# Optimization experiments

Hardware: AMD Instinct MI355X
Metric: run time of the kernel (lower is better)

## Reference

```python
import jax, jax.numpy as jnp
import numpy as np

GROUPS = 32
EPS = 1e-3  # keras GroupNormalization default epsilon


def setup_inputs() -> dict:
    key = jax.random.key(0)
    ks = jax.random.split(key, 7)
    B, H, W, C = 16, 32, 32, 512
    inputs = jax.random.normal(ks[0], (B, H, W, C), dtype=jnp.float32)
    gamma = jnp.ones((C,), dtype=jnp.float32)
    beta = jnp.zeros((C,), dtype=jnp.float32)
    # EinsumDense 'bhwc,cae->bhwae', output last dims (C,3), bias axes 'ae'
    W_qkv = jax.random.normal(ks[1], (C, C, 3), dtype=jnp.float32) / np.sqrt(C)
    b_qkv = jnp.zeros((C, 3), dtype=jnp.float32)
    # EinsumDense 'bhwc,cd->bhwd', bias axes 'd'
    W_out = jax.random.normal(ks[2], (C, C), dtype=jnp.float32) / np.sqrt(C)
    b_out = jnp.zeros((C,), dtype=jnp.float32)
    return {
        "inputs": inputs,
        "gamma": gamma,
        "beta": beta,
        "W_qkv": W_qkv,
        "b_qkv": b_qkv,
        "W_out": W_out,
        "b_out": b_out,
    }


def group_norm(x, gamma, beta):
    B, H, W, C = x.shape
    g = GROUPS
    xr = x.reshape(B, H, W, g, C // g)
    mean = jnp.mean(xr, axis=(1, 2, 4), keepdims=True)
    var = jnp.var(xr, axis=(1, 2, 4), keepdims=True)
    xn = (xr - mean) * jax.lax.rsqrt(var + EPS)
    return xn.reshape(B, H, W, C) * gamma + beta


def reference(inputs, gamma, beta, W_qkv, b_qkv, W_out, b_out):
    B, H, W, C = inputs.shape
    scale = C ** (-0.5)
    x = group_norm(inputs, gamma, beta)
    # QKV projection: bhwc,cae->bhwae  (+ bias over 'ae')
    qkv = jnp.einsum("bhwc,cae->bhwae", x, W_qkv) + b_qkv
    q, k, v = qkv[..., 0], qkv[..., 1], qkv[..., 2]  # each [B,H,W,C]
    # full spatial attention: [B,H,W,H,W]
    attn = jnp.einsum("bhwc,btlc->bhwtl", q, k) * scale
    attn = attn.reshape(B, H, W, H * W)
    attn = jax.nn.softmax(attn, axis=-1)
    attn = attn.reshape(B, H, W, H, W)
    out = jnp.einsum("bhwtl,btlc->bhwc", attn, v)
    out = jnp.einsum("bhwc,cd->bhwd", out, W_out) + b_out
    return inputs + out
```

## Files before the change

### kernel.cpp

```cpp
#include <hip/hip_runtime.h>
#include <hip/hip_bf16.h>

#define NB    16
#define SP    1024
#define NC    512
#define NG    32
#define MTOT  (NB*SP)
#define EPSV  1e-3f
#define SCALE 0.04419417382415922f

using f32x4   = __attribute__((ext_vector_type(4))) float;
using short8  = __attribute__((ext_vector_type(8))) short;
using short4v = __attribute__((ext_vector_type(4))) short;
using bf16x8v = __attribute__((ext_vector_type(8))) __bf16;

__device__ __forceinline__ unsigned short f2bf(float f) {
  union { float f; unsigned int u; } x; x.f = f;
  unsigned int u = x.u;
  unsigned int r = (u + 0x7FFFu + ((u >> 16) & 1u)) >> 16;
  return (unsigned short)r;
}
__device__ __forceinline__ float bf2f(unsigned short b) {
  union { unsigned int u; float f; } x; x.u = ((unsigned int)b) << 16;
  return x.f;
}

#define GLOAD_LDS16(g, l)                                                     \
  __builtin_amdgcn_global_load_lds(                                           \
      (const __attribute__((address_space(1))) void*)(g),                     \
      (__attribute__((address_space(3))) void*)(l), 16, 0, 0)

__global__ __launch_bounds__(256) void gn_stats_k(const float* __restrict__ x,
                                                  float2* __restrict__ stats) {
  int bg = blockIdx.x;
  int b = bg >> 5, g = bg & 31;
  int tid = threadIdx.x;
  int c = tid & 15, s0 = tid >> 4;
  const float* base = x + (long)b * SP * NC + g * 16 + c;
  float s = 0.f, ss = 0.f;
  for (int sp = s0; sp < SP; sp += 16) {
    float v = base[(long)sp * NC];
    s += v; ss += v * v;
  }
  for (int o = 32; o > 0; o >>= 1) { s += __shfl_xor(s, o); ss += __shfl_xor(ss, o); }
  __shared__ float rs[4], rss[4];
  int lane = tid & 63, wv = tid >> 6;
  if (lane == 0) { rs[wv] = s; rss[wv] = ss; }
  __syncthreads();
  if (tid == 0) {
    float S = rs[0] + rs[1] + rs[2] + rs[3];
    float SS = rss[0] + rss[1] + rss[2] + rss[3];
    float mean = S * (1.f / 16384.f);
    float var  = SS * (1.f / 16384.f) - mean * mean;
    stats[bg] = make_float2(mean, rsqrtf(var + EPSV));
  }
}

__global__ __launch_bounds__(256) void gn_apply_k(const float* __restrict__ x,
                                                  const float2* __restrict__ stats,
                                                  const float* __restrict__ gamma,
                                                  const float* __restrict__ beta,
                                                  unsigned short* __restrict__ xn) {
  long t = (long)blockIdx.x * 256 + threadIdx.x;
  long base = t * 8;
  int c = (int)(base & 511);
  int b = (int)(base >> 19);
  float2 st = stats[b * NG + (c >> 4)];
  f32x4 v0 = *reinterpret_cast<const f32x4*>(x + base);
  f32x4 v1 = *reinterpret_cast<const f32x4*>(x + base + 4);
  f32x4 g0 = *reinterpret_cast<const f32x4*>(gamma + c);
  f32x4 g1 = *reinterpret_cast<const f32x4*>(gamma + c + 4);
  f32x4 b0 = *reinterpret_cast<const f32x4*>(beta + c);
  f32x4 b1 = *reinterpret_cast<const f32x4*>(beta + c + 4);
  short8 o;
  #pragma unroll
  for (int q = 0; q < 4; ++q) {
    float sc = st.y * g0[q];
    o[q] = (short)f2bf(v0[q] * sc + (b0[q] - st.x * sc));
  }
  #pragma unroll
  for (int q = 0; q < 4; ++q) {
    float sc = st.y * g1[q];
    o[q + 4] = (short)f2bf(v1[q] * sc + (b1[q] - st.x * sc));
  }
  *reinterpret_cast<short8*>(xn + base) = o;
}

__global__ __launch_bounds__(256) void pack_wqkv_k(const float* __restrict__ W,
                                                   const float* __restrict__ bq,
                                                   unsigned short* __restrict__ Wp,
                                                   float* __restrict__ bp) {
  int idx = blockIdx.x * 256 + threadIdx.x;
  int n = idx >> 9, c = idx & 511;
  int e = n >> 9, a = n & 511;
  Wp[idx] = f2bf(W[((long)c * 512 + a) * 3 + e]);
  if (idx < 1536) {
    int e2 = idx >> 9, a2 = idx & 511;
    bp[idx] = bq[a2 * 3 + e2];
  }
}

__global__ __launch_bounds__(256) void pack_wout_k(const float* __restrict__ W,
                                                   unsigned short* __restrict__ Wp) {
  int idx = blockIdx.x * 256 + threadIdx.x;
  int n = idx >> 9, c = idx & 511;
  Wp[idx] = f2bf(W[(long)c * 512 + n]);
}

__global__ void transpose_v_k(const unsigned short* __restrict__ qkv,
                              unsigned short* __restrict__ vT) {
  __shared__ unsigned short t[32][33];
  int bs = blockIdx.x, bc = blockIdx.y, b = blockIdx.z;
  int tx = threadIdx.x, ty = threadIdx.y;
  #pragma unroll
  for (int k = 0; k < 4; ++k) {
    int s = bs * 32 + ty + k * 8, c = bc * 32 + tx;
    t[ty + k * 8][tx] = qkv[((long)b * SP + s) * 1536 + 1024 + c];
  }
  __syncthreads();
  #pragma unroll
  for (int k = 0; k < 4; ++k) {
    int c = bc * 32 + ty + k * 8, s = bs * 32 + tx;
    vT[((long)b * NC + c) * SP + s] = t[tx][ty + k * 8];
  }
}

__global__ __launch_bounds__(256) void softmax_k(unsigned short* __restrict__ S) {
  long row = blockIdx.x;
  unsigned short* r = S + row * 1024;
  int tid = threadIdx.x, lane = tid & 63, wv = tid >> 6;
  short4v raw = *reinterpret_cast<const short4v*>(r + tid * 4);
  float v[4];
  #pragma unroll
  for (int q = 0; q < 4; ++q) v[q] = bf2f((unsigned short)raw[q]);
  float m = fmaxf(fmaxf(v[0], v[1]), fmaxf(v[2], v[3]));
  for (int o = 32; o > 0; o >>= 1) m = fmaxf(m, __shfl_xor(m, o));
  __shared__ float wm[4], ws[4];
  if (lane == 0) wm[wv] = m;
  __syncthreads();
  float rmax = fmaxf(fmaxf(wm[0], wm[1]), fmaxf(wm[2], wm[3]));
  float e[4]; float ssum = 0.f;
  #pragma unroll
  for (int q = 0; q < 4; ++q) { e[q] = __expf(v[q] - rmax); ssum += e[q]; }
  for (int o = 32; o > 0; o >>= 1) ssum += __shfl_xor(ssum, o);
  if (lane == 0) ws[wv] = ssum;
  __syncthreads();
  float inv = 1.f / (ws[0] + ws[1] + ws[2] + ws[3]);
  short4v pv;
  #pragma unroll
  for (int q = 0; q < 4; ++q) pv[q] = (short)f2bf(e[q] * inv);
  *reinterpret_cast<short4v*>(r + tid * 4) = pv;
}

template <int EPI>
__global__ __launch_bounds__(256) void gemm_tn(
    const unsigned short* __restrict__ Ap, long strideA, int lda,
    const unsigned short* __restrict__ Bp, long strideB, int ldb,
    void* __restrict__ Op, long strideO, int ldo,
    const float* __restrict__ bias, const float* __restrict__ residual,
    int K, float scale) {
  __shared__ unsigned short As[128 * 32];
  __shared__ unsigned short Bs[128 * 32];
  const int tid = threadIdx.x;
  const int lane = tid & 63, wv = tid >> 6;

  const int nwg  = gridDim.x * gridDim.y;
  const int flat = blockIdx.y * gridDim.x + blockIdx.x;
  const int w    = (flat & 7) * (nwg >> 3) + (flat >> 3);
  const int bn = (w % gridDim.x) * 128;
  const int bm = (w / gridDim.x) * 128;
  const int z = blockIdx.z;
  const unsigned short* Ag = Ap + (long)z * strideA;
  const unsigned short* Bg = Bp + (long)z * strideB;

  const int srow = lane >> 2;
  const int scol = (lane & 3) * 8;
  const int wm = (wv >> 1) * 64, wn = (wv & 1) * 64;
  const int lrow = lane & 15, lk = (lane >> 4) * 8;

  f32x4 acc[4][4] = {};
  for (int kt = 0; kt < K; kt += 32) {
    #pragma unroll
    for (int it = 0; it < 2; ++it) {
      int chunk = it * 4 + wv;
      int row = chunk * 16 + srow;
      GLOAD_LDS16(Ag + (long)(bm + row) * lda + kt + scol, As + chunk * 512);
      GLOAD_LDS16(Bg + (long)(bn + row) * ldb + kt + scol, Bs + chunk * 512);
    }
    __syncthreads();

    short8 afr[4], bfr[4];
    #pragma unroll
    for (int i = 0; i < 4; ++i)
      afr[i] = *reinterpret_cast<const short8*>(&As[(wm + i * 16 + lrow) * 32 + lk]);
    #pragma unroll
    for (int j = 0; j < 4; ++j)
      bfr[j] = *reinterpret_cast<const short8*>(&Bs[(wn + j * 16 + lrow) * 32 + lk]);
    #pragma unroll
    for (int i = 0; i < 4; ++i)
      #pragma unroll
      for (int j = 0; j < 4; ++j)
        acc[i][j] = __builtin_amdgcn_mfma_f32_16x16x32_bf16(
            __builtin_bit_cast(bf16x8v, afr[i]),
            __builtin_bit_cast(bf16x8v, bfr[j]), acc[i][j], 0, 0, 0);
    __syncthreads();
  }

  const int colb = bn + wn + (lane & 15);
  #pragma unroll
  for (int i = 0; i < 4; ++i) {
    #pragma unroll
    for (int r = 0; r < 4; ++r) {
      int rowg = bm + wm + i * 16 + (lane >> 4) * 4 + r;
      #pragma unroll
      for (int j = 0; j < 4; ++j) {
        int colg = colb + j * 16;
        float v = acc[i][j][r];
        if (EPI == 0) {
          v += bias[colg];
          ((unsigned short*)Op)[(long)z * strideO + (long)rowg * ldo + colg] = f2bf(v);
        } else if (EPI == 2) {
          ((unsigned short*)Op)[(long)z * strideO + (long)rowg * ldo + colg] = f2bf(v * scale);
        } else {
          v += bias[colg] + residual[(long)rowg * ldo + colg];
          ((float*)Op)[(long)rowg * ldo + colg] = v;
        }
      }
    }
  }
}

extern "C" void kernel_launch(void* const* d_in, const int* in_sizes, int n_in,
                              void* d_out, int out_size, void* d_ws, size_t ws_size,
                              hipStream_t stream) {
  const float* x     = (const float*)d_in[0];
  const float* gamma = (const float*)d_in[1];
  const float* beta  = (const float*)d_in[2];
  const float* Wqkv  = (const float*)d_in[3];
  const float* bqkv  = (const float*)d_in[4];
  const float* Wout  = (const float*)d_in[5];
  const float* bout  = (const float*)d_in[6];
  float* out = (float*)d_out;

  char* ws = (char*)d_ws;
  float2*         stats = (float2*)(ws + 0);
  unsigned short* wqkvP = (unsigned short*)(ws + 4096);
  float*          bqP   = (float*)(ws + 1576960);
  unsigned short* woutT = (unsigned short*)(ws + 1583104);
  unsigned short* qkv   = (unsigned short*)(ws + 2107392);
  unsigned short* vT    = (unsigned short*)(ws + 52439040);
  unsigned short* Sbuf  = (unsigned short*)(ws + 69216256);
  unsigned short* attn  = (unsigned short*)(ws + 136325120);
  unsigned short* xn    = (unsigned short*)(ws + 153102336);

  gn_stats_k<<<512, 256, 0, stream>>>(x, stats);
  gn_apply_k<<<4096, 256, 0, stream>>>(x, stats, gamma, beta, xn);
  pack_wqkv_k<<<3072, 256, 0, stream>>>(Wqkv, bqkv, wqkvP, bqP);
  pack_wout_k<<<1024, 256, 0, stream>>>(Wout, woutT);

  gemm_tn<0><<<dim3(12, 128, 1), 256, 0, stream>>>(
      xn, 0L, NC, wqkvP, 0L, NC, qkv, 0L, 1536,
      bqP, nullptr, NC, 1.f);

  transpose_v_k<<<dim3(32, 16, 16), dim3(32, 8), 0, stream>>>(qkv, vT);

  gemm_tn<2><<<dim3(8, 8, 16), 256, 0, stream>>>(
      qkv, (long)SP * 1536, 1536, qkv + 512, (long)SP * 1536, 1536,
      Sbuf, (long)SP * SP, SP, nullptr, nullptr, NC, SCALE);

  softmax_k<<<MTOT, 256, 0, stream>>>(Sbuf);

  gemm_tn<2><<<dim3(4, 8, 16), 256, 0, stream>>>(
      Sbuf, (long)SP * SP, SP, vT, (long)NC * SP, SP,
      attn, (long)SP * NC, NC, nullptr, nullptr, SP, 1.f);

  gemm_tn<3><<<dim3(4, 128, 1), 256, 0, stream>>>(
      attn, 0L, NC, woutT, 0L, NC, out, 0L, NC,
      bout, x, NC, 1.f);
}
```

Measured before the change: 291.8 us.

## Replace GEMM with 8-wave 128x256 tile, 4-stage LDS pipeline and swizzle

```diff
diff --git a/kernel.cpp b/kernel.cpp
--- a/kernel.cpp
+++ b/kernel.cpp
@@ -153,65 +153,110 @@
 }
 
 template <int EPI>
-__global__ __launch_bounds__(256) void gemm_tn(
+__global__ __launch_bounds__(512, 2) void gemm8(
     const unsigned short* __restrict__ Ap, long strideA, int lda,
     const unsigned short* __restrict__ Bp, long strideB, int ldb,
     void* __restrict__ Op, long strideO, int ldo,
     const float* __restrict__ bias, const float* __restrict__ residual,
     int K, float scale) {
-  __shared__ unsigned short As[128 * 32];
-  __shared__ unsigned short Bs[128 * 32];
+  constexpr int SLOT = 24576;
+  extern __shared__ unsigned char smem[];
   const int tid = threadIdx.x;
   const int lane = tid & 63, wv = tid >> 6;
+  const int wm2 = wv >> 2, wn4 = wv & 3;
 
   const int nwg  = gridDim.x * gridDim.y;
   const int flat = blockIdx.y * gridDim.x + blockIdx.x;
   const int w    = (flat & 7) * (nwg >> 3) + (flat >> 3);
-  const int bn = (w % gridDim.x) * 128;
+  const int bn = (w % gridDim.x) * 256;
   const int bm = (w / gridDim.x) * 128;
   const int z = blockIdx.z;
   const unsigned short* Ag = Ap + (long)z * strideA;
   const unsigned short* Bg = Bp + (long)z * strideB;
 
-  const int srow = lane >> 2;
-  const int scol = (lane & 3) * 8;
-  const int wm = (wv >> 1) * 64, wn = (wv & 1) * 64;
-  const int lrow = lane & 15, lk = (lane >> 4) * 8;
+  long offA;
+  { int sid = tid, sr = sid >> 3, sl = (sid & 7) ^ (sr & 7);
+    offA = (long)(bm + sr * 2 + (sl >> 2)) * lda + (sl & 3) * 8; }
+  long offB0, offB1;
+  { int sid = tid, sr = sid >> 3, sl = (sid & 7) ^ (sr & 7);
+    offB0 = (long)(bn + sr * 2 + (sl >> 2)) * ldb + (sl & 3) * 8;
+    sid = 512 + tid; sr = sid >> 3; sl = (sid & 7) ^ (sr & 7);
+    offB1 = (long)(bn + sr * 2 + (sl >> 2)) * ldb + (sl & 3) * 8; }
+  const int ldsA_off  = wv * 1024;
+  const int ldsB0_off = 8192 + wv * 1024;
+  const int ldsB1_off = 16384 + wv * 1024;
+
+  int aoff[4], boff[4];
+  #pragma unroll
+  for (int i = 0; i < 4; ++i) {
+    int r = wm2 * 64 + i * 16 + (lane & 15);
+    int sr = r >> 1, sl = ((r & 1) * 4 + (lane >> 4)) ^ (sr & 7);
+    aoff[i] = sr * 128 + sl * 16;
+  }
+  #pragma unroll
+  for (int j = 0; j < 4; ++j) {
+    int r = wn4 * 64 + j * 16 + (lane & 15);
+    int sr = r >> 1, sl = ((r & 1) * 4 + (lane >> 4)) ^ (sr & 7);
+    boff[j] = 8192 + sr * 128 + sl * 16;
+  }
+
+  const int NT = K >> 5;
+  #pragma unroll
+  for (int t = 0; t < 3; ++t) {
+    int sb = t * SLOT, kt = t * 32;
+    GLOAD_LDS16(Ag + offA + kt,  smem + sb + ldsA_off);
+    GLOAD_LDS16(Bg + offB0 + kt, smem + sb + ldsB0_off);
+    GLOAD_LDS16(Bg + offB1 + kt, smem + sb + ldsB1_off);
+  }
+  asm volatile("s_waitcnt vmcnt(6)" ::: "memory");
+  __builtin_amdgcn_s_barrier();
 
   f32x4 acc[4][4] = {};
-  for (int kt = 0; kt < K; kt += 32) {
-    #pragma unroll
-    for (int it = 0; it < 2; ++it) {
-      int chunk = it * 4 + wv;
-      int row = chunk * 16 + srow;
-      GLOAD_LDS16(Ag + (long)(bm + row) * lda + kt + scol, As + chunk * 512);
-      GLOAD_LDS16(Bg + (long)(bn + row) * ldb + kt + scol, Bs + chunk * 512);
-    }
-    __syncthreads();
-
-    short8 afr[4], bfr[4];
+  for (int t = 0; t < NT; ++t) {
+    const unsigned char* sa = smem + (t & 3) * SLOT;
+    short8 av[4], bv[4];
     #pragma unroll
     for (int i = 0; i < 4; ++i)
-      afr[i] = *reinterpret_cast<const short8*>(&As[(wm + i * 16 + lrow) * 32 + lk]);
+      av[i] = *reinterpret_cast<const short8*>(sa + aoff[i]);
     #pragma unroll
     for (int j = 0; j < 4; ++j)
-      bfr[j] = *reinterpret_cast<const short8*>(&Bs[(wn + j * 16 + lrow) * 32 + lk]);
+      bv[j] = *reinterpret_cast<const short8*>(sa + boff[j]);
+    if (t + 3 < NT) {
+      int sb = ((t + 3) & 3) * SLOT, kt = (t + 3) * 32;
+      GLOAD_LDS16(Ag + offA + kt,  smem + sb + ldsA_off);
+      GLOAD_LDS16(Bg + offB0 + kt, smem + sb + ldsB0_off);
+      GLOAD_LDS16(Bg + offB1 + kt, smem + sb + ldsB1_off);
+    }
+    __builtin_amdgcn_s_barrier();
+    asm volatile("s_waitcnt lgkmcnt(0)" ::: "memory");
+    __builtin_amdgcn_sched_barrier(0);
+    __builtin_amdgcn_s_setprio(1);
     #pragma unroll
     for (int i = 0; i < 4; ++i)
       #pragma unroll
       for (int j = 0; j < 4; ++j)
         acc[i][j] = __builtin_amdgcn_mfma_f32_16x16x32_bf16(
-            __builtin_bit_cast(bf16x8v, afr[i]),
-            __builtin_bit_cast(bf16x8v, bfr[j]), acc[i][j], 0, 0, 0);
-    __syncthreads();
-  }
-
-  const int colb = bn + wn + (lane & 15);
+            __builtin_bit_cast(bf16x8v, av[i]),
+            __builtin_bit_cast(bf16x8v, bv[j]), acc[i][j], 0, 0, 0);
+    __builtin_amdgcn_s_setprio(0);
+    __builtin_amdgcn_sched_barrier(0);
+    if (t + 3 < NT) {
+      asm volatile("s_waitcnt vmcnt(6)" ::: "memory");
+    } else if (t + 2 < NT) {
+      asm volatile("s_waitcnt vmcnt(3)" ::: "memory");
+    } else {
+      asm volatile("s_waitcnt vmcnt(0)" ::: "memory");
+    }
+    __builtin_amdgcn_s_barrier();
+  }
+
+  const int colb = bn + wn4 * 64 + (lane & 15);
+  const int rowb = bm + wm2 * 64 + (lane >> 4) * 4;
   #pragma unroll
   for (int i = 0; i < 4; ++i) {
     #pragma unroll
     for (int r = 0; r < 4; ++r) {
-      int rowg = bm + wm + i * 16 + (lane >> 4) * 4 + r;
+      int rowg = rowb + i * 16 + r;
       #pragma unroll
       for (int j = 0; j < 4; ++j) {
         int colg = colb + j * 16;
@@ -253,28 +298,35 @@
   unsigned short* attn  = (unsigned short*)(ws + 136325120);
   unsigned short* xn    = (unsigned short*)(ws + 153102336);
 
+  (void)hipFuncSetAttribute((const void*)gemm8<0>,
+        hipFuncAttributeMaxDynamicSharedMemorySize, 98304);
+  (void)hipFuncSetAttribute((const void*)gemm8<2>,
+        hipFuncAttributeMaxDynamicSharedMemorySize, 98304);
+  (void)hipFuncSetAttribute((const void*)gemm8<3>,
+        hipFuncAttributeMaxDynamicSharedMemorySize, 98304);
+
   gn_stats_k<<<512, 256, 0, stream>>>(x, stats);
   gn_apply_k<<<4096, 256, 0, stream>>>(x, stats, gamma, beta, xn);
   pack_wqkv_k<<<3072, 256, 0, stream>>>(Wqkv, bqkv, wqkvP, bqP);
   pack_wout_k<<<1024, 256, 0, stream>>>(Wout, woutT);
 
-  gemm_tn<0><<<dim3(12, 128, 1), 256, 0, stream>>>(
+  gemm8<0><<<dim3(6, 128, 1), 512, 98304, stream>>>(
       xn, 0L, NC, wqkvP, 0L, NC, qkv, 0L, 1536,
       bqP, nullptr, NC, 1.f);
 
   transpose_v_k<<<dim3(32, 16, 16), dim3(32, 8), 0, stream>>>(qkv, vT);
 
-  gemm_tn<2><<<dim3(8, 8, 16), 256, 0, stream>>>(
+  gemm8<2><<<dim3(4, 8, 16), 512, 98304, stream>>>(
       qkv, (long)SP * 1536, 1536, qkv + 512, (long)SP * 1536, 1536,
       Sbuf, (long)SP * SP, SP, nullptr, nullptr, NC, SCALE);
 
   softmax_k<<<MTOT, 256, 0, stream>>>(Sbuf);
 
-  gemm_tn<2><<<dim3(4, 8, 16), 256, 0, stream>>>(
+  gemm8<2><<<dim3(2, 8, 16), 512, 98304, stream>>>(
       Sbuf, (long)SP * SP, SP, vT, (long)NC * SP, SP,
       attn, (long)SP * NC, NC, nullptr, nullptr, SP, 1.f);
 
-  gemm_tn<3><<<dim3(4, 128, 1), 256, 0, stream>>>(
+  gemm8<3><<<dim3(2, 128, 1), 512, 98304, stream>>>(
       attn, 0L, NC, woutT, 0L, NC, out, 0L, NC,
       bout, x, NC, 1.f);
 }
```

New measurement: 279.6 us. -4.2%, faster.
